# Kernel tuning notes

Measured on AMD Instinct MI355X. Metric: run time of the kernel, lower is better.

## Reference

```python
import jax, jax.numpy as jnp
import numpy as np

N_EMB = 512
EMB_DIM = 64
BETA = 0.25


def setup_inputs() -> dict:
    key = jax.random.key(0)
    k1, k2 = jax.random.split(key)
    z = jax.random.normal(k1, (32, EMB_DIM, 64, 64), dtype=jnp.float32)
    # nn.Embedding weight init: uniform(-1/n_embeddings, 1/n_embeddings)
    codebook = jax.random.uniform(k2, (N_EMB, EMB_DIM), dtype=jnp.float32,
                                  minval=-1.0 / N_EMB, maxval=1.0 / N_EMB)
    return {"z": z, "codebook": codebook}


def reference(z, codebook):
    # z: [B, C, H, W] -> [B, H, W, C]
    z_nhwc = jnp.transpose(z, (0, 2, 3, 1))
    B, H, W, C = z_nhwc.shape
    zf = z_nhwc.reshape(-1, C)  # [N, C]
    # squared L2 distances to each code: ||z||^2 + ||e||^2 - 2 z.e
    dist = (jnp.sum(zf * zf, axis=1, keepdims=True)
            + jnp.sum(codebook * codebook, axis=1)
            - 2.0 * jnp.matmul(zf, codebook.T))  # [N, n_emb]
    indices = jnp.argmin(dist, axis=1)  # [N]
    # one-hot @ codebook == gather (same math, efficient form)
    z_q = codebook[indices].reshape(B, H, W, C)
    embedding_loss = jnp.mean((jax.lax.stop_gradient(z_q) - z_nhwc) ** 2)
    # straight-through estimator
    z_q_st = z_nhwc + jax.lax.stop_gradient(z_q - z_nhwc)
    z_q_out = jnp.transpose(z_q_st, (0, 3, 1, 2))  # back to [B, C, H, W]
    return (embedding_loss, z_q_out, indices)
```

## Files before the change

### kernel.cpp

```cpp
#include <hip/hip_runtime.h>


#define C_DIM   64
#define N_EMB   512
#define HW      4096
#define N_PIX   (32 * HW)
#define ZQ_OFF  1
#define IDX_OFF (1 + N_PIX * C_DIM)
#define NBLK    512
#define TPB     1024

typedef _Float16 half8 __attribute__((ext_vector_type(8)));
typedef float    f32x4 __attribute__((ext_vector_type(4)));
union FragH { unsigned u[4]; half8 h8; uint4 u4; _Float16 h[8]; };

__device__ __forceinline__ unsigned umn(unsigned a, unsigned b){ return a<b?a:b; }
__device__ __forceinline__ unsigned umx(unsigned a, unsigned b){ return a>b?a:b; }
__device__ __forceinline__ unsigned med3u(unsigned a, unsigned b, unsigned c){
    unsigned r;
    asm("v_med3_u32 %0, %1, %2, %3" : "=v"(r) : "v"(a), "v"(b), "v"(c));
    return r;
}

__global__ __launch_bounds__(TPB, 4) void vq_main(
    const float* __restrict__ z,
    const float* __restrict__ cb,
    float* __restrict__ out,
    float* __restrict__ ws)
{
    __shared__ unsigned cbh[N_EMB * 32];
    __shared__ float    esh5[N_EMB];
    __shared__ float    eshx[N_EMB];
    __shared__ float    wsum[16];

    const int t = threadIdx.x;

    if (t < N_EMB) {
        const float* e = cb + t * C_DIM;
        float ev[64];
        #pragma unroll
        for (int q = 0; q < 16; ++q) {
            float4 v = ((const float4*)e)[q];
            ev[4*q+0]=v.x; ev[4*q+1]=v.y; ev[4*q+2]=v.z; ev[4*q+3]=v.w;
        }
        float r[8];
        #pragma unroll
        for (int i = 0; i < 8; ++i) r[i] = __fmul_rn(ev[i], ev[i]);
        #pragma unroll
        for (int k = 8; k < 64; k += 8) {
            #pragma unroll
            for (int i = 0; i < 8; ++i)
                r[i] = __fadd_rn(r[i], __fmul_rn(ev[k+i], ev[k+i]));
        }
        float es = __fadd_rn(
            __fadd_rn(__fadd_rn(r[0],r[1]), __fadd_rn(r[2],r[3])),
            __fadd_rn(__fadd_rn(r[4],r[5]), __fadd_rn(r[6],r[7])));
        eshx[t] = es;
        esh5[t] = __fmul_rn(__fadd_rn(es, 0.5f), 256.0f);
        unsigned hw_[32];
        #pragma unroll
        for (int w2 = 0; w2 < 32; ++w2) {
            union { _Float16 hh[2]; unsigned u; } pk;
            pk.hh[0] = (_Float16)(ev[2*w2]   * -512.0f);
            pk.hh[1] = (_Float16)(ev[2*w2+1] * -512.0f);
            hw_[w2] = pk.u;
        }
        const int rs = t & 7;
        #pragma unroll
        for (int g = 0; g < 8; ++g) {
            int g2 = g ^ rs;
            *(uint4*)&cbh[t*32 + g2*4] =
                make_uint4(hw_[4*g], hw_[4*g+1], hw_[4*g+2], hw_[4*g+3]);
        }
    }
    __syncthreads();

    const int l   = t & 63;
    const int wv  = t >> 6;
    const int lg  = l >> 4;
    const int li  = l & 15;
    const int bb  = blockIdx.x >> 4;
    const int g20 = (lg)     ^ (li & 7);
    const int g21 = (4 + lg) ^ (li & 7);
    const int jb  = lg * 4;
    float ls = 0.f;

    const int pxw = blockIdx.x * 256 + wv * 16 + li;
    const float* zb = z + (size_t)bb * (C_DIM * HW) + (pxw & (HW - 1));

    FragH b0, b1;
    float apx = 0.f;
    {
        const float* c0 = zb + (size_t)(lg*8) * HW;
        const float* c1 = zb + (size_t)(32 + lg*8) * HW;
        #pragma unroll
        for (int i = 0; i < 8; ++i) {
            float x0 = c0[(size_t)i*HW], x1 = c1[(size_t)i*HW];
            b0.h[i] = (_Float16)x0;
            b1.h[i] = (_Float16)x1;
            apx = __fmaf_rn(x0, x0, apx);
            apx = __fmaf_rn(x1, x1, apx);
        }
        apx += __shfl_xor(apx, 16, 64);
        apx += __shfl_xor(apx, 32, 64);
    }

    unsigned s1[4], s2[4], s3[4];
    #pragma unroll
    for (int i = 0; i < 4; ++i) { s1[i]=0xFFFFFFFFu; s2[i]=0xFFFFFFFFu; s3[i]=0xFFFFFFFFu; }
    #pragma unroll 4
    for (int T = 0; T < 32; ++T) {
        const int row = T*16 + li;
        FragH a0, a1;
        a0.u4 = *(const uint4*)&cbh[row*32 + g20*4];
        a1.u4 = *(const uint4*)&cbh[row*32 + g21*4];
        f32x4 acc = *(const f32x4*)&esh5[T*16 + jb];
        acc = __builtin_amdgcn_mfma_f32_16x16x32_f16(a0.h8, b0.h8, acc, 0,0,0);
        acc = __builtin_amdgcn_mfma_f32_16x16x32_f16(a1.h8, b1.h8, acc, 0,0,0);
        const int jT = T*16 + jb;
        #pragma unroll
        for (int r2 = 0; r2 < 4; ++r2) {
            unsigned key = (__float_as_uint(acc[r2]) & 0xFFFFFE00u) | (unsigned)(jT + r2);
            unsigned nk3 = med3u(key, s2[r2], s3[r2]);
            unsigned nk2 = med3u(key, s1[r2], s2[r2]);
            s1[r2] = umn(s1[r2], key); s2[r2] = nk2; s3[r2] = nk3;
        }
    }

    unsigned m1, m2;
    {
        unsigned p1 = umn(s1[0], s1[1]);
        unsigned p2 = umn(umx(s1[0], s1[1]), umn(s2[0], s2[1]));
        unsigned q1 = umn(s1[2], s1[3]);
        unsigned q2 = umn(umx(s1[2], s1[3]), umn(s2[2], s2[3]));
        m1 = umn(p1, q1);
        m2 = umn(umx(p1, q1), umn(p2, q2));
        #pragma unroll
        for (int m = 16; m <= 32; m <<= 1) {
            unsigned o1 = __shfl_xor(m1, m, 64), o2 = __shfl_xor(m2, m, 64);
            unsigned nm2 = umn(umx(m1, o1), umn(m2, o2));
            m1 = umn(m1, o1); m2 = nm2;
        }
    }
    const float d1m = __uint_as_float(m1 & 0xFFFFFE00u);
    const float d2m = __uint_as_float(m2 & 0xFFFFFE00u);
    const bool  amb = (d2m - d1m) <= 0.030720f;

    int bj;
    if (__ballot(amb) == 0ULL) {
        bj = (int)(m1 & 511u);
        if (l < 16) {
            out[IDX_OFF + pxw] = (float)bj;
            float dd = __uint_as_float((m1 & 0xFFFFFE00u) | 0x100u);
            ls += __fmaf_rn(dd, 0.00390625f, apx - 0.5f);
        }
    } else {
        unsigned k1, k2, k3;
        {
            #define MERGE3(o1,o2,o3, a1,a2,a3, b1,b2,b3)                     \
                o1 = umn(a1, b1);                                            \
                o2 = med3u(a1, b1, umn(a2, b2));                             \
                o3 = umn(umn(a3, b3), umn(umx(a2, b1), umx(a1, b2)));
            unsigned x1,x2,x3, y1,y2,y3;
            MERGE3(x1,x2,x3, s1[0],s2[0],s3[0], s1[1],s2[1],s3[1]);
            MERGE3(y1,y2,y3, s1[2],s2[2],s3[2], s1[3],s2[3],s3[3]);
            MERGE3(k1,k2,k3, x1,x2,x3, y1,y2,y3);
            #undef MERGE3
        }
        float zr[64];
        #pragma unroll
        for (int c = 0; c < 64; ++c) zr[c] = zb[(size_t)c * HW];
        float ap;
        {
            float r[8];
            #pragma unroll
            for (int i = 0; i < 8; ++i) r[i] = __fmul_rn(zr[i], zr[i]);
            #pragma unroll
            for (int k = 8; k < 64; k += 8) {
                #pragma unroll
                for (int i = 0; i < 8; ++i)
                    r[i] = __fadd_rn(r[i], __fmul_rn(zr[k+i], zr[k+i]));
            }
            ap = __fadd_rn(
                __fadd_rn(__fadd_rn(r[0],r[1]), __fadd_rn(r[2],r[3])),
                __fadd_rn(__fadd_rn(r[4],r[5]), __fadd_rn(r[6],r[7])));
        }
        const float thr = d1m + 0.030720f;
        float bd = 3.0e38f; bj = 1023;

        #define RESCORE(K) do {                                               \
            float da_ = __uint_as_float((K) & 0xFFFFFE00u);                   \
            if (da_ <= thr) {                                                 \
                int j_ = (int)((K) & 511u);                                   \
                const float* er_ = cb + (size_t)j_ * 64;                      \
                float a_ = 0.f;                                               \
                _Pragma("unroll")                                             \
                for (int c_ = 0; c_ < 64; ++c_)                               \
                    a_ = __fmaf_rn(zr[c_], er_[c_], a_);                      \
                float dd_ = __fsub_rn(__fadd_rn(ap, eshx[j_]),                \
                                      __fmul_rn(2.0f, a_));                   \
                if (dd_ < bd || (dd_ == bd && j_ < bj)) { bd = dd_; bj = j_; }\
            }                                                                 \
        } while (0)
        RESCORE(k1); RESCORE(k2); RESCORE(k3);
        #undef RESCORE

        #pragma unroll
        for (int m = 16; m <= 32; m <<= 1) {
            float od = __shfl_xor(bd, m, 64);
            int   oj = __shfl_xor(bj, m, 64);
            if (od < bd || (od == bd && oj < bj)) { bd = od; bj = oj; }
        }
        if (l < 16) {
            out[IDX_OFF + pxw] = (float)bj;
            ls += bd;
        }
    }

    {
        const int cq = l >> 4;
        const float* eb = cb + (size_t)bj * 64;
        float* zq = out + ZQ_OFF + (size_t)bb * (C_DIM * HW) + (pxw & (HW - 1));
        #pragma unroll
        for (int cc = 0; cc < 16; ++cc) {
            int c = cq * 16 + cc;
            zq[(size_t)c * HW] = eb[c];
        }
    }

    #pragma unroll
    for (int off = 32; off; off >>= 1) ls += __shfl_down(ls, off, 64);
    if (l == 0) wsum[wv] = ls;
    __syncthreads();
    if (t == 0) {
        float s = 0.f;
        #pragma unroll
        for (int i = 0; i < 16; ++i) s += wsum[i];
        ws[blockIdx.x] = s;
    }
}

__global__ __launch_bounds__(256) void vq_loss(
    const float* __restrict__ ws, float* __restrict__ out)
{
    __shared__ float sm[4];
    float v = ws[threadIdx.x] + ws[threadIdx.x + 256];
    #pragma unroll
    for (int off = 32; off; off >>= 1) v += __shfl_down(v, off, 64);
    const int lane = threadIdx.x & 63, wid = threadIdx.x >> 6;
    if (lane == 0) sm[wid] = v;
    __syncthreads();
    if (threadIdx.x == 0)
        out[0] = ((sm[0] + sm[1]) + (sm[2] + sm[3])) * (1.0f / 8388608.0f);
}

extern "C" void kernel_launch(void* const* d_in, const int* in_sizes, int n_in,
                              void* d_out, int out_size, void* d_ws, size_t ws_size,
                              hipStream_t stream)
{
    const float* z  = (const float*)d_in[0];
    const float* cb = (const float*)d_in[1];
    float* out = (float*)d_out;
    float* ws  = (float*)d_ws;

    vq_main<<<NBLK, TPB, 0, stream>>>(z, cb, out, ws);
    vq_loss<<<1, 256, 0, stream>>>(ws, out);
}
```

Measured before the change: 42.12 us.

## Process two 16-pixel tiles per wave to reuse codebook fragments across MFMAs

The block shrinks from 1024 to 512 threads, and each wave now handles 32 pixels as two B fragments that share each codebook A fragment loaded from LDS. This halves the LDS codebook reads per pixel and interleaves independent MFMA chains, at the cost of more registers for the doubled top-3 state. The z_q store is reorganised so each lane writes 32 channels for one of 32 pixels, using shuffles to distribute the chosen indices. The codebook preload now runs on all 512 threads, with no t<N_EMB guard.

```diff
diff --git a/kernel.cpp b/kernel.cpp
--- a/kernel.cpp
+++ b/kernel.cpp
@@ -8,7 +8,7 @@
 #define ZQ_OFF  1
 #define IDX_OFF (1 + N_PIX * C_DIM)
 #define NBLK    512
-#define TPB     1024
+#define TPB     512
 
 typedef _Float16 half8 __attribute__((ext_vector_type(8)));
 typedef float    f32x4 __attribute__((ext_vector_type(4)));
@@ -31,11 +31,11 @@
     __shared__ unsigned cbh[N_EMB * 32];
     __shared__ float    esh5[N_EMB];
     __shared__ float    eshx[N_EMB];
-    __shared__ float    wsum[16];
+    __shared__ float    wsum[8];
 
     const int t = threadIdx.x;
 
-    if (t < N_EMB) {
+    {
         const float* e = cb + t * C_DIM;
         float ev[64];
         #pragma unroll
@@ -85,145 +85,175 @@
     const int jb  = lg * 4;
     float ls = 0.f;
 
-    const int pxw = blockIdx.x * 256 + wv * 16 + li;
-    const float* zb = z + (size_t)bb * (C_DIM * HW) + (pxw & (HW - 1));
-
-    FragH b0, b1;
-    float apx = 0.f;
+    const int pxw0 = blockIdx.x * 256 + wv * 32;
+    const float* zbA = z + (size_t)bb * (C_DIM * HW) + ((pxw0      + li) & (HW-1));
+    const float* zbB = z + (size_t)bb * (C_DIM * HW) + ((pxw0 + 16 + li) & (HW-1));
+
+    FragH bA0, bA1, bB0, bB1;
+    float apxA = 0.f, apxB = 0.f;
     {
-        const float* c0 = zb + (size_t)(lg*8) * HW;
-        const float* c1 = zb + (size_t)(32 + lg*8) * HW;
+        const float* c0 = zbA + (size_t)(lg*8) * HW;
+        const float* c1 = zbA + (size_t)(32 + lg*8) * HW;
+        const float* c2 = zbB + (size_t)(lg*8) * HW;
+        const float* c3 = zbB + (size_t)(32 + lg*8) * HW;
         #pragma unroll
         for (int i = 0; i < 8; ++i) {
             float x0 = c0[(size_t)i*HW], x1 = c1[(size_t)i*HW];
-            b0.h[i] = (_Float16)x0;
-            b1.h[i] = (_Float16)x1;
-            apx = __fmaf_rn(x0, x0, apx);
-            apx = __fmaf_rn(x1, x1, apx);
-        }
-        apx += __shfl_xor(apx, 16, 64);
-        apx += __shfl_xor(apx, 32, 64);
-    }
-
-    unsigned s1[4], s2[4], s3[4];
-    #pragma unroll
-    for (int i = 0; i < 4; ++i) { s1[i]=0xFFFFFFFFu; s2[i]=0xFFFFFFFFu; s3[i]=0xFFFFFFFFu; }
+            float y0 = c2[(size_t)i*HW], y1 = c3[(size_t)i*HW];
+            bA0.h[i] = (_Float16)x0;  bA1.h[i] = (_Float16)x1;
+            bB0.h[i] = (_Float16)y0;  bB1.h[i] = (_Float16)y1;
+            apxA = __fmaf_rn(x0, x0, apxA); apxA = __fmaf_rn(x1, x1, apxA);
+            apxB = __fmaf_rn(y0, y0, apxB); apxB = __fmaf_rn(y1, y1, apxB);
+        }
+        apxA += __shfl_xor(apxA, 16, 64);  apxA += __shfl_xor(apxA, 32, 64);
+        apxB += __shfl_xor(apxB, 16, 64);  apxB += __shfl_xor(apxB, 32, 64);
+    }
+
+    unsigned sA1[4], sA2[4], sA3[4], sB1[4], sB2[4], sB3[4];
+    #pragma unroll
+    for (int i = 0; i < 4; ++i) {
+        sA1[i]=sA2[i]=sA3[i]=0xFFFFFFFFu;
+        sB1[i]=sB2[i]=sB3[i]=0xFFFFFFFFu;
+    }
     #pragma unroll 4
     for (int T = 0; T < 32; ++T) {
         const int row = T*16 + li;
         FragH a0, a1;
         a0.u4 = *(const uint4*)&cbh[row*32 + g20*4];
         a1.u4 = *(const uint4*)&cbh[row*32 + g21*4];
-        f32x4 acc = *(const f32x4*)&esh5[T*16 + jb];
-        acc = __builtin_amdgcn_mfma_f32_16x16x32_f16(a0.h8, b0.h8, acc, 0,0,0);
-        acc = __builtin_amdgcn_mfma_f32_16x16x32_f16(a1.h8, b1.h8, acc, 0,0,0);
+        f32x4 es = *(const f32x4*)&esh5[T*16 + jb];
+        f32x4 accA = es, accB = es;
+        accA = __builtin_amdgcn_mfma_f32_16x16x32_f16(a0.h8, bA0.h8, accA, 0,0,0);
+        accB = __builtin_amdgcn_mfma_f32_16x16x32_f16(a0.h8, bB0.h8, accB, 0,0,0);
+        accA = __builtin_amdgcn_mfma_f32_16x16x32_f16(a1.h8, bA1.h8, accA, 0,0,0);
+        accB = __builtin_amdgcn_mfma_f32_16x16x32_f16(a1.h8, bB1.h8, accB, 0,0,0);
         const int jT = T*16 + jb;
         #pragma unroll
         for (int r2 = 0; r2 < 4; ++r2) {
-            unsigned key = (__float_as_uint(acc[r2]) & 0xFFFFFE00u) | (unsigned)(jT + r2);
-            unsigned nk3 = med3u(key, s2[r2], s3[r2]);
-            unsigned nk2 = med3u(key, s1[r2], s2[r2]);
-            s1[r2] = umn(s1[r2], key); s2[r2] = nk2; s3[r2] = nk3;
-        }
-    }
-
-    unsigned m1, m2;
+            unsigned keyA = (__float_as_uint(accA[r2]) & 0xFFFFFE00u) | (unsigned)(jT + r2);
+            unsigned keyB = (__float_as_uint(accB[r2]) & 0xFFFFFE00u) | (unsigned)(jT + r2);
+            unsigned nA3 = med3u(keyA, sA2[r2], sA3[r2]);
+            unsigned nA2 = med3u(keyA, sA1[r2], sA2[r2]);
+            sA1[r2] = umn(sA1[r2], keyA); sA2[r2] = nA2; sA3[r2] = nA3;
+            unsigned nB3 = med3u(keyB, sB2[r2], sB3[r2]);
+            unsigned nB2 = med3u(keyB, sB1[r2], sB2[r2]);
+            sB1[r2] = umn(sB1[r2], keyB); sB2[r2] = nB2; sB3[r2] = nB3;
+        }
+    }
+
+    int bjA, bjB;
+    #pragma unroll
+    for (int pt = 0; pt < 2; ++pt) {
+        unsigned (&s1)[4] = pt ? sB1 : sA1;
+        unsigned (&s2)[4] = pt ? sB2 : sA2;
+        unsigned (&s3)[4] = pt ? sB3 : sA3;
+        const float* zb = pt ? zbB : zbA;
+        const float apx = pt ? apxB : apxA;
+        const int   px  = pxw0 + pt*16 + li;
+
+        unsigned m1, m2;
+        {
+            unsigned p1 = umn(s1[0], s1[1]);
+            unsigned p2 = umn(umx(s1[0], s1[1]), umn(s2[0], s2[1]));
+            unsigned q1 = umn(s1[2], s1[3]);
+            unsigned q2 = umn(umx(s1[2], s1[3]), umn(s2[2], s2[3]));
+            m1 = umn(p1, q1);
+            m2 = umn(umx(p1, q1), umn(p2, q2));
+            #pragma unroll
+            for (int m = 16; m <= 32; m <<= 1) {
+                unsigned o1 = __shfl_xor(m1, m, 64), o2 = __shfl_xor(m2, m, 64);
+                unsigned nm2 = umn(umx(m1, o1), umn(m2, o2));
+                m1 = umn(m1, o1); m2 = nm2;
+            }
+        }
+        const float d1m = __uint_as_float(m1 & 0xFFFFFE00u);
+        const float d2m = __uint_as_float(m2 & 0xFFFFFE00u);
+        const bool  amb = (d2m - d1m) <= 0.030720f;
+
+        int bj;
+        if (__ballot(amb) == 0ULL) {
+            bj = (int)(m1 & 511u);
+            if (l < 16) {
+                out[IDX_OFF + px] = (float)bj;
+                float dd = __uint_as_float((m1 & 0xFFFFFE00u) | 0x100u);
+                ls += __fmaf_rn(dd, 0.00390625f, apx - 0.5f);
+            }
+        } else {
+            unsigned k1, k2, k3;
+            {
+                #define MERGE3(o1,o2,o3, a1,a2,a3, b1,b2,b3)                 \
+                    o1 = umn(a1, b1);                                        \
+                    o2 = med3u(a1, b1, umn(a2, b2));                         \
+                    o3 = umn(umn(a3, b3), umn(umx(a2, b1), umx(a1, b2)));
+                unsigned x1,x2,x3, y1,y2,y3;
+                MERGE3(x1,x2,x3, s1[0],s2[0],s3[0], s1[1],s2[1],s3[1]);
+                MERGE3(y1,y2,y3, s1[2],s2[2],s3[2], s1[3],s2[3],s3[3]);
+                MERGE3(k1,k2,k3, x1,x2,x3, y1,y2,y3);
+                #undef MERGE3
+            }
+            float zr[64];
+            #pragma unroll
+            for (int c = 0; c < 64; ++c) zr[c] = zb[(size_t)c * HW];
+            float ap;
+            {
+                float r[8];
+                #pragma unroll
+                for (int i = 0; i < 8; ++i) r[i] = __fmul_rn(zr[i], zr[i]);
+                #pragma unroll
+                for (int k = 8; k < 64; k += 8) {
+                    #pragma unroll
+                    for (int i = 0; i < 8; ++i)
+                        r[i] = __fadd_rn(r[i], __fmul_rn(zr[k+i], zr[k+i]));
+                }
+                ap = __fadd_rn(
+                    __fadd_rn(__fadd_rn(r[0],r[1]), __fadd_rn(r[2],r[3])),
+                    __fadd_rn(__fadd_rn(r[4],r[5]), __fadd_rn(r[6],r[7])));
+            }
+            const float thr = d1m + 0.030720f;
+            float bd = 3.0e38f; bj = 1023;
+
+            #define RESCORE(K) do {                                               \
+                float da_ = __uint_as_float((K) & 0xFFFFFE00u);                   \
+                if (da_ <= thr) {                                                 \
+                    int j_ = (int)((K) & 511u);                                   \
+                    const float* er_ = cb + (size_t)j_ * 64;                      \
+                    float a_ = 0.f;                                               \
+                    _Pragma("unroll")                                             \
+                    for (int c_ = 0; c_ < 64; ++c_)                               \
+                        a_ = __fmaf_rn(zr[c_], er_[c_], a_);                      \
+                    float dd_ = __fsub_rn(__fadd_rn(ap, eshx[j_]),                \
+                                          __fmul_rn(2.0f, a_));                   \
+                    if (dd_ < bd || (dd_ == bd && j_ < bj)) { bd = dd_; bj = j_; }\
+                }                                                                 \
+            } while (0)
+            RESCORE(k1); RESCORE(k2); RESCORE(k3);
+            #undef RESCORE
+
+            #pragma unroll
+            for (int m = 16; m <= 32; m <<= 1) {
+                float od = __shfl_xor(bd, m, 64);
+                int   oj = __shfl_xor(bj, m, 64);
+                if (od < bd || (od == bd && oj < bj)) { bd = od; bj = oj; }
+            }
+            if (l < 16) {
+                out[IDX_OFF + px] = (float)bj;
+                ls += bd;
+            }
+        }
+        if (pt == 0) bjA = bj; else bjB = bj;
+    }
+
     {
-        unsigned p1 = umn(s1[0], s1[1]);
-        unsigned p2 = umn(umx(s1[0], s1[1]), umn(s2[0], s2[1]));
-        unsigned q1 = umn(s1[2], s1[3]);
-        unsigned q2 = umn(umx(s1[2], s1[3]), umn(s2[2], s2[3]));
-        m1 = umn(p1, q1);
-        m2 = umn(umx(p1, q1), umn(p2, q2));
-        #pragma unroll
-        for (int m = 16; m <= 32; m <<= 1) {
-            unsigned o1 = __shfl_xor(m1, m, 64), o2 = __shfl_xor(m2, m, 64);
-            unsigned nm2 = umn(umx(m1, o1), umn(m2, o2));
-            m1 = umn(m1, o1); m2 = nm2;
-        }
-    }
-    const float d1m = __uint_as_float(m1 & 0xFFFFFE00u);
-    const float d2m = __uint_as_float(m2 & 0xFFFFFE00u);
-    const bool  amb = (d2m - d1m) <= 0.030720f;
-
-    int bj;
-    if (__ballot(amb) == 0ULL) {
-        bj = (int)(m1 & 511u);
-        if (l < 16) {
-            out[IDX_OFF + pxw] = (float)bj;
-            float dd = __uint_as_float((m1 & 0xFFFFFE00u) | 0x100u);
-            ls += __fmaf_rn(dd, 0.00390625f, apx - 0.5f);
-        }
-    } else {
-        unsigned k1, k2, k3;
-        {
-            #define MERGE3(o1,o2,o3, a1,a2,a3, b1,b2,b3)                     \
-                o1 = umn(a1, b1);                                            \
-                o2 = med3u(a1, b1, umn(a2, b2));                             \
-                o3 = umn(umn(a3, b3), umn(umx(a2, b1), umx(a1, b2)));
-            unsigned x1,x2,x3, y1,y2,y3;
-            MERGE3(x1,x2,x3, s1[0],s2[0],s3[0], s1[1],s2[1],s3[1]);
-            MERGE3(y1,y2,y3, s1[2],s2[2],s3[2], s1[3],s2[3],s3[3]);
-            MERGE3(k1,k2,k3, x1,x2,x3, y1,y2,y3);
-            #undef MERGE3
-        }
-        float zr[64];
-        #pragma unroll
-        for (int c = 0; c < 64; ++c) zr[c] = zb[(size_t)c * HW];
-        float ap;
-        {
-            float r[8];
-            #pragma unroll
-            for (int i = 0; i < 8; ++i) r[i] = __fmul_rn(zr[i], zr[i]);
-            #pragma unroll
-            for (int k = 8; k < 64; k += 8) {
-                #pragma unroll
-                for (int i = 0; i < 8; ++i)
-                    r[i] = __fadd_rn(r[i], __fmul_rn(zr[k+i], zr[k+i]));
-            }
-            ap = __fadd_rn(
-                __fadd_rn(__fadd_rn(r[0],r[1]), __fadd_rn(r[2],r[3])),
-                __fadd_rn(__fadd_rn(r[4],r[5]), __fadd_rn(r[6],r[7])));
-        }
-        const float thr = d1m + 0.030720f;
-        float bd = 3.0e38f; bj = 1023;
-
-        #define RESCORE(K) do {                                               \
-            float da_ = __uint_as_float((K) & 0xFFFFFE00u);                   \
-            if (da_ <= thr) {                                                 \
-                int j_ = (int)((K) & 511u);                                   \
-                const float* er_ = cb + (size_t)j_ * 64;                      \
-                float a_ = 0.f;                                               \
-                _Pragma("unroll")                                             \
-                for (int c_ = 0; c_ < 64; ++c_)                               \
-                    a_ = __fmaf_rn(zr[c_], er_[c_], a_);                      \
-                float dd_ = __fsub_rn(__fadd_rn(ap, eshx[j_]),                \
-                                      __fmul_rn(2.0f, a_));                   \
-                if (dd_ < bd || (dd_ == bd && j_ < bj)) { bd = dd_; bj = j_; }\
-            }                                                                 \
-        } while (0)
-        RESCORE(k1); RESCORE(k2); RESCORE(k3);
-        #undef RESCORE
-
-        #pragma unroll
-        for (int m = 16; m <= 32; m <<= 1) {
-            float od = __shfl_xor(bd, m, 64);
-            int   oj = __shfl_xor(bj, m, 64);
-            if (od < bd || (od == bd && oj < bj)) { bd = od; bj = oj; }
-        }
-        if (l < 16) {
-            out[IDX_OFF + pxw] = (float)bj;
-            ls += bd;
-        }
-    }
-
-    {
-        const int cq = l >> 4;
-        const float* eb = cb + (size_t)bj * 64;
-        float* zq = out + ZQ_OFF + (size_t)bb * (C_DIM * HW) + (pxw & (HW - 1));
-        #pragma unroll
-        for (int cc = 0; cc < 16; ++cc) {
-            int c = cq * 16 + cc;
+        const int pm  = l & 31;
+        const int hh  = l >> 5;
+        int b0 = __shfl(bjA, pm & 15, 64);
+        int b1 = __shfl(bjB, pm & 15, 64);
+        const int bjw = (pm >> 4) ? b1 : b0;
+        const float* eb = cb + (size_t)bjw * 64;
+        float* zq = out + ZQ_OFF + (size_t)bb * (C_DIM * HW) + ((pxw0 + pm) & (HW-1));
+        #pragma unroll
+        for (int cc = 0; cc < 32; ++cc) {
+            int c = hh * 32 + cc;
             zq[(size_t)c * HW] = eb[c];
         }
     }
@@ -235,7 +265,7 @@
     if (t == 0) {
         float s = 0.f;
         #pragma unroll
-        for (int i = 0; i < 16; ++i) s += wsum[i];
+        for (int i = 0; i < 8; ++i) s += wsum[i];
         ws[blockIdx.x] = s;
     }
 }
```

Measured after the change: 40.35 us, median of 2. 1.04x faster.
